# Performance work log

Measured on AMD Instinct MI355X. Metric: run time of the kernel, lower is better.

Reference implementation:

```python
import jax, jax.numpy as jnp
import numpy as np

C, S, D, H, FF = 8, 512, 512, 8, 2048
DH = D // H
N = C * S
NUM_SAMPLES = 4
SEG_LEN = N // NUM_SAMPLES  # 2 channels * 512 tokens per sample


def _ln(x, w, b):
    m = x.mean(-1, keepdims=True)
    v = ((x - m) ** 2).mean(-1, keepdims=True)
    return (x - m) / jnp.sqrt(v + 1e-5) * w + b


def _rope_1d(t, p, inv_freq):
    # t: (H, N, hd), p: (N,), inv_freq: (hd//2,)
    f = p[:, None] * inv_freq[None, :]          # (N, hd//2)
    emb = jnp.concatenate([f, f], -1)           # (N, hd)
    cos, sin = jnp.cos(emb), jnp.sin(emb)
    half = t.shape[-1] // 2
    rot = jnp.concatenate([-t[..., half:], t[..., :half]], -1)
    return t * cos + rot * sin


def setup_inputs() -> dict:
    key = jax.random.key(0)
    ks = jax.random.split(key, 8)
    s = 0.02
    return {
        "x": jax.random.normal(ks[0], (C, S, D), jnp.float32),
        "pos": jax.random.uniform(ks[1], (C, S, 2), jnp.float32) * 100.0,
        "mask": jnp.zeros((C, S), jnp.bool_),
        "seg_ids": jnp.arange(N, dtype=jnp.int32),
        "Wqkv": jax.random.normal(ks[2], (D, 3 * D), jnp.float32) * s,
        "bqkv": jnp.zeros((3 * D,), jnp.float32),
        "Wo": jax.random.normal(ks[3], (D, D), jnp.float32) * s,
        "bo": jnp.zeros((D,), jnp.float32),
        "ln1_w": jnp.ones((D,), jnp.float32),
        "ln1_b": jnp.zeros((D,), jnp.float32),
        "ln2_w": jnp.ones((D,), jnp.float32),
        "ln2_b": jnp.zeros((D,), jnp.float32),
        "W1": jax.random.normal(ks[4], (D, FF), jnp.float32) * s,
        "b1": jnp.zeros((FF,), jnp.float32),
        "W2": jax.random.normal(ks[5], (FF, D), jnp.float32) * s,
        "b2": jnp.zeros((D,), jnp.float32),
    }


def reference(x, pos, mask, seg_ids, Wqkv, bqkv, Wo, bo,
              ln1_w, ln1_b, ln2_w, ln2_b, W1, b1, W2, b2):
    # Zero-mask forward_cc path: all C*S tokens are packed into one varlen batch.
    xf = x.reshape(N, D)
    pf = pos.reshape(N, 2)
    seg = seg_ids // SEG_LEN  # segment id per token (cu_seq_len semantics)

    # --- pre-LN MHA with 2D axial RoPE ---
    hn = _ln(xf, ln1_w, ln1_b)
    qkv = hn @ Wqkv + bqkv
    q, k, v = jnp.split(qkv, 3, axis=-1)
    to_heads = lambda t: t.reshape(N, H, DH).transpose(1, 0, 2)  # (H, N, DH)
    q, k, v = to_heads(q), to_heads(k), to_heads(v)

    hd2 = DH // 2
    inv_freq = 1.0 / (10000.0 ** (jnp.arange(0, hd2, 2, dtype=jnp.float32) / hd2))

    def rope2d(t):
        a = _rope_1d(t[..., :hd2], pf[:, 0], inv_freq)
        b = _rope_1d(t[..., hd2:], pf[:, 1], inv_freq)
        return jnp.concatenate([a, b], -1)

    q, k = rope2d(q), rope2d(k)

    scores = jnp.einsum('hnd,hmd->hnm', q, k) / np.float32(np.sqrt(DH))
    allowed = seg[:, None] == seg[None, :]  # block-diagonal varlen mask
    scores = jnp.where(allowed[None], scores, jnp.float32(-1e30))
    attn = jax.nn.softmax(scores, axis=-1)
    o = jnp.einsum('hnm,hmd->hnd', attn, v).transpose(1, 0, 2).reshape(N, D)
    h = xf + (o @ Wo + bo)

    # --- pre-LN FFN ---
    hn2 = _ln(h, ln2_w, ln2_b)
    h = h + (jax.nn.gelu(hn2 @ W1 + b1) @ W2 + b2)
    return h.reshape(C, S, D)
```

## Files before the change

### kernel.cpp

```cpp
#include <hip/hip_runtime.h>
#include <hip/hip_bf16.h>


typedef __hip_bfloat16 bf16;
typedef float f4 __attribute__((ext_vector_type(4)));
typedef short short8 __attribute__((ext_vector_type(8)));

#define C_ 8
#define S_ 512
#define D_ 512
#define H_ 8
#define DH_ 64
#define FF_ 2048
#define N_ 4096
#define SEGLEN 1024

__device__ __forceinline__ float bfbits2f(unsigned short u) {
    return __uint_as_float(((unsigned)u) << 16);
}
__device__ __forceinline__ unsigned short f2bfbits(float f) {
    __hip_bfloat16 h = __float2bfloat16(f);
    return *reinterpret_cast<unsigned short*>(&h);
}
__device__ __forceinline__ float in_get(const void* p, int i, int isbf) {
    return isbf ? bfbits2f(((const unsigned short*)p)[i]) : ((const float*)p)[i];
}
__device__ __forceinline__ int probe_bf(const void* ln1w) {
    return ((const unsigned*)ln1w)[0] != 0x3F800000u;
}
__device__ __forceinline__ float gelu_f(float x) {
    float u = 0.7978845608028654f * fmaf(0.044715f * x, x * x, x);
    return 0.5f * x * (1.0f + tanhf(u));
}
__device__ __forceinline__ void gl2lds16(const void* g, void* l) {
    __builtin_amdgcn_global_load_lds(
        (const __attribute__((address_space(1))) void*)g,
        (__attribute__((address_space(3))) void*)l, 16, 0, 0);
}

__device__ __forceinline__ void ln_row(
    const void* in, const void* w, const void* b, unsigned short* out,
    int isbf, int row, int lane, int in_fp32)
{
    int base = row * D_ + lane * 8;
    float v[8];
    if (in_fp32 || !isbf) {
        const f4* p = (const f4*)((const float*)in + base);
        f4 x0 = p[0], x1 = p[1];
        v[0] = x0[0]; v[1] = x0[1]; v[2] = x0[2]; v[3] = x0[3];
        v[4] = x1[0]; v[5] = x1[1]; v[6] = x1[2]; v[7] = x1[3];
    } else {
        uint4 u = *(const uint4*)((const unsigned short*)in + base);
        unsigned uu[4] = {u.x, u.y, u.z, u.w};
        #pragma unroll
        for (int j = 0; j < 4; j++) {
            v[2 * j]     = __uint_as_float(uu[j] << 16);
            v[2 * j + 1] = __uint_as_float(uu[j] & 0xFFFF0000u);
        }
    }
    float s = 0.f, q = 0.f;
    #pragma unroll
    for (int j = 0; j < 8; j++) { s += v[j]; q = fmaf(v[j], v[j], q); }
    #pragma unroll
    for (int m = 32; m; m >>= 1) { s += __shfl_xor(s, m); q += __shfl_xor(q, m); }
    float mean = s * (1.f / D_);
    float var  = q * (1.f / D_) - mean * mean;
    float rstd = rsqrtf(var + 1e-5f);
    unsigned short o[8];
    #pragma unroll
    for (int j = 0; j < 8; j++) {
        float wj = in_get(w, lane * 8 + j, isbf);
        float bj = in_get(b, lane * 8 + j, isbf);
        o[j] = f2bfbits((v[j] - mean) * rstd * wj + bj);
    }
    uint4 uo;
    uo.x = o[0] | ((unsigned)o[1] << 16);
    uo.y = o[2] | ((unsigned)o[3] << 16);
    uo.z = o[4] | ((unsigned)o[5] << 16);
    uo.w = o[6] | ((unsigned)o[7] << 16);
    *(uint4*)(out + base) = uo;
}

__global__ __launch_bounds__(256) void prep_kernel(
    const void* __restrict__ Wqkv, const void* __restrict__ Wo,
    const void* __restrict__ W1,   const void* __restrict__ W2,
    bf16* __restrict__ WqkvT, bf16* __restrict__ WoT,
    bf16* __restrict__ W1T,   bf16* __restrict__ W2T,
    const void* __restrict__ x, const void* __restrict__ ln1w,
    const void* __restrict__ ln1b, unsigned short* __restrict__ hn)
{
    const int isbf = probe_bf(ln1w);
    __shared__ unsigned short t2[64 * 40];
    int b = blockIdx.x;
    if (b < 1536) {
        const void* src; bf16* dst; int K, N, nt, kt;
        if (b < 384)       { src = Wqkv; dst = WqkvT; K = 512;  N = 1536; nt = b % 24;          kt = b / 24; }
        else if (b < 512)  { src = Wo;   dst = WoT;   K = 512;  N = 512;  nt = (b - 384) % 8;   kt = (b - 384) / 8; }
        else if (b < 1024) { src = W1;   dst = W1T;   K = 512;  N = 2048; nt = (b - 512) % 32;  kt = (b - 512) / 32; }
        else               { src = W2;   dst = W2T;   K = 2048; N = 512;  nt = (b - 1024) % 8;  kt = (b - 1024) / 8; }
        int nb = nt * 64, kb = kt * 32;
        #pragma unroll
        for (int pass = 0; pass < 2; pass++) {
            int k = pass * 16 + (threadIdx.x >> 4);
            int n = (threadIdx.x & 15) * 4;
            size_t gidx = (size_t)(kb + k) * N + nb + n;
            unsigned short v[4];
            if (!isbf) {
                f4 xv = *(const f4*)((const float*)src + gidx);
                v[0] = f2bfbits(xv[0]); v[1] = f2bfbits(xv[1]);
                v[2] = f2bfbits(xv[2]); v[3] = f2bfbits(xv[3]);
            } else {
                ushort4 u = *(const ushort4*)((const unsigned short*)src + gidx);
                v[0] = u.x; v[1] = u.y; v[2] = u.z; v[3] = u.w;
            }
            #pragma unroll
            for (int e = 0; e < 4; e++) t2[(n + e) * 40 + k] = v[e];
        }
        __syncthreads();
        int n = threadIdx.x >> 2, kc = (threadIdx.x & 3) * 8;
        uint4 w = *(const uint4*)&t2[n * 40 + kc];
        *(uint4*)&((unsigned short*)dst)[(size_t)(nb + n) * K + kb + kc] = w;
    } else {
        int row = (b - 1536) * 4 + (threadIdx.x >> 6);
        ln_row(x, ln1w, ln1b, hn, isbf, row, threadIdx.x & 63, 0);
    }
}

__global__ __launch_bounds__(256) void ln_kernel(
    const void* __restrict__ in, const void* __restrict__ w, const void* __restrict__ b,
    unsigned short* __restrict__ out, const void* __restrict__ dtp, int in_fp32)
{
    const int isbf = probe_bf(dtp);
    int row = blockIdx.x * 4 + (threadIdx.x >> 6);
    ln_row(in, w, b, out, isbf, row, threadIdx.x & 63, in_fp32);
}

template<int MODE, int TN>
__global__ __launch_bounds__(256) void gemm_kernel(
    const bf16* __restrict__ A, const bf16* __restrict__ Bt,
    const void* __restrict__ bias, const void* __restrict__ res,
    const void* __restrict__ pos,
    void* __restrict__ out0, void* __restrict__ out1,
    int K, int NN, const void* __restrict__ dtp)
{
    const int isbf = probe_bf(dtp);
    constexpr int AS = 64 * 64;
    constexpr int BS = TN * 64;
    constexpr int BUF = AS + BS;
    constexpr int VTSZ = 128 * 72;
    constexpr int SMSZ = (2 * BUF > VTSZ) ? 2 * BUF : VTSZ;
    __shared__ __align__(16) unsigned short smem[SMSZ];
    const int X = blockIdx.x & 7, jj = blockIdx.x >> 3;
    const int m0 = ((jj / NN) * 8 + X) * 64;
    const int n0 = (jj % NN) * TN;
    const int tid = threadIdx.x;
    const int wave = tid >> 6, lane = tid & 63;
    const int quad = lane >> 4, l16 = lane & 15;
    const int wr = wave >> 1, wc = wave & 1;
    constexpr int NT = TN / 32;
    constexpr int NB = TN / 32;

    const bf16* gA[2]; int dA[2];
    const bf16* gB[NB]; int dB[NB];
    #pragma unroll
    for (int j = 0; j < 2; j++) {
        int s = j * 256 + tid;
        int r = s >> 3, cc = ((s & 7) - r) & 7;
        gA[j] = A + (size_t)(m0 + r) * K + cc * 8;
        dA[j] = (j * 256 + wave * 64) * 8;
    }
    #pragma unroll
    for (int j = 0; j < NB; j++) {
        int s = j * 256 + tid;
        int r = s >> 3, cc = ((s & 7) - r) & 7;
        gB[j] = Bt + (size_t)(n0 + r) * K + cc * 8;
        dB[j] = (j * 256 + wave * 64) * 8;
    }
    auto stage = [&](int b, int kt) {
        unsigned short* Ab = smem + b * BUF;
        unsigned short* Bb = Ab + AS;
        #pragma unroll
        for (int j = 0; j < 2; j++) gl2lds16(gA[j] + kt * 64, Ab + dA[j]);
        #pragma unroll
        for (int j = 0; j < NB; j++) gl2lds16(gB[j] + kt * 64, Bb + dB[j]);
    };

    f4 acc[2][NT] = {};
    const int nk = K >> 6;
    stage(0, 0);
    #pragma unroll 1
    for (int kt = 0; kt < nk; kt++) {
        const int cur = kt & 1;
        __syncthreads();
        if (kt + 1 < nk) stage(cur ^ 1, kt + 1);
        const unsigned short* Ab = smem + cur * BUF;
        const unsigned short* Bb = Ab + AS;
        short8 af[2][2], bfr[NT][2];
        #pragma unroll
        for (int mi = 0; mi < 2; mi++) {
            int r = wr * 32 + mi * 16 + l16;
            #pragma unroll
            for (int h = 0; h < 2; h++)
                af[mi][h] = *(const short8*)&Ab[(r * 8 + ((h * 4 + quad + r) & 7)) * 8];
        }
        #pragma unroll
        for (int ni = 0; ni < NT; ni++) {
            int r = wc * (TN / 2) + ni * 16 + l16;
            #pragma unroll
            for (int h = 0; h < 2; h++)
                bfr[ni][h] = *(const short8*)&Bb[(r * 8 + ((h * 4 + quad + r) & 7)) * 8];
        }
        #pragma unroll
        for (int mi = 0; mi < 2; mi++)
            #pragma unroll
            for (int ni = 0; ni < NT; ni++) {
                acc[mi][ni] = __builtin_amdgcn_mfma_f32_16x16x32_bf16(af[mi][0], bfr[ni][0], acc[mi][ni], 0, 0, 0);
                acc[mi][ni] = __builtin_amdgcn_mfma_f32_16x16x32_bf16(af[mi][1], bfr[ni][1], acc[mi][ni], 0, 0, 0);
            }
    }

    const int colbase = n0 + wc * (TN / 2);
    float bb[NT];
    #pragma unroll
    for (int ni = 0; ni < NT; ni++) bb[ni] = in_get(bias, colbase + ni * 16 + l16, isbf);

    if (MODE == 1) {
        const int tsel = colbase >> 9;
        const int hd = (colbase & 511) >> 6;
        if (tsel < 2) {
            unsigned short* out = (unsigned short*)out0 + ((size_t)(tsel * H_ + hd) * N_) * 64;
            const float invf = __expf(-(float)l16 * 0.5756462732485114f);
            const float qscale = (tsel == 0) ? 0.125f : 1.0f;
            #pragma unroll
            for (int half = 0; half < 2; half++) {
                #pragma unroll
                for (int mi = 0; mi < 2; mi++) {
                    #pragma unroll
                    for (int r = 0; r < 4; r++) {
                        int row = m0 + wr * 32 + mi * 16 + quad * 4 + r;
                        float p = in_get(pos, row * 2 + half, isbf);
                        float sn, cs;
                        __sincosf(p * invf, &sn, &cs);
                        float v0 = acc[mi][half * 2][r]     + bb[half * 2];
                        float v1 = acc[mi][half * 2 + 1][r] + bb[half * 2 + 1];
                        out[(size_t)row * 64 + half * 32 + l16]      = f2bfbits((v0 * cs - v1 * sn) * qscale);
                        out[(size_t)row * 64 + half * 32 + 16 + l16] = f2bfbits((v1 * cs + v0 * sn) * qscale);
                    }
                }
            }
        } else {
            __syncthreads();
            unsigned short* VT = smem;
            const int vd_blk = n0 - 1024;
            #pragma unroll
            for (int mi = 0; mi < 2; mi++)
                #pragma unroll
                for (int ni = 0; ni < NT; ni++) {
                    int vd = wc * 64 + ni * 16 + l16;
                    #pragma unroll
                    for (int r = 0; r < 4; r++) {
                        int tok = wr * 32 + mi * 16 + quad * 4 + r;
                        VT[vd * 72 + tok] = f2bfbits(acc[mi][ni][r] + bb[ni]);
                    }
                }
            __syncthreads();
            unsigned short* vt = (unsigned short*)out1;
            #pragma unroll
            for (int j = 0; j < 4; j++) {
                int cch = j * 256 + tid;
                int dim = cch >> 3, tc = cch & 7;
                uint4 v = *(const uint4*)&VT[dim * 72 + tc * 8];
                *(uint4*)&vt[(size_t)(vd_blk + dim) * N_ + m0 + tc * 8] = v;
            }
        }
    } else {
        #pragma unroll
        for (int mi = 0; mi < 2; mi++)
            #pragma unroll
            for (int ni = 0; ni < NT; ni++) {
                int col = colbase + ni * 16 + l16;
                #pragma unroll
                for (int r = 0; r < 4; r++) {
                    int row = m0 + wr * 32 + mi * 16 + quad * 4 + r;
                    float val = acc[mi][ni][r] + bb[ni];
                    if (MODE == 2) {
                        size_t idx = (size_t)row * D_ + col;
                        ((float*)out0)[idx] = val + in_get(res, idx, isbf);
                    } else if (MODE == 3) {
                        ((unsigned short*)out0)[(size_t)row * FF_ + col] = f2bfbits(gelu_f(val));
                    } else {
                        size_t idx = (size_t)row * D_ + col;
                        float o = val + ((const float*)res)[idx];
                        if (isbf) ((unsigned short*)out0)[idx] = f2bfbits(o);
                        else      ((float*)out0)[idx] = o;
                    }
                }
            }
    }
}

#define PSTR 136
__global__ __launch_bounds__(256) void attn_kernel(
    const unsigned short* __restrict__ QKb, const unsigned short* __restrict__ Vt,
    unsigned short* __restrict__ ob)
{
    __shared__ __align__(16) unsigned short Ksm[128 * 64];
    __shared__ __align__(16) unsigned short Vsm[64 * 128];
    __shared__ __align__(16) unsigned short Psm[4][16 * PSTR];
    const int h = blockIdx.x & 7, jb = blockIdx.x >> 3;
    const int sg = jb >> 4, qt = jb & 15;
    const int tid = threadIdx.x;
    const int wave = tid >> 6, lane = tid & 63;
    const int quad = lane >> 4, l16 = lane & 15;
    const unsigned short* Qg = QKb + ((size_t)h * N_ + sg * SEGLEN + qt * 64 + wave * 16) * 64;
    const unsigned short* Kg = QKb + ((size_t)(H_ + h) * N_ + sg * SEGLEN) * 64;
    const unsigned short* Vg = Vt + (size_t)h * 64 * N_ + sg * SEGLEN;
    unsigned short* Pw = Psm[wave];

    const unsigned short* gK[4];
    const unsigned short* gV[4];
    unsigned short* lK[4];
    unsigned short* lV[4];
    #pragma unroll
    for (int j = 0; j < 4; j++) {
        int s = j * 256 + tid;
        int rk = s >> 3, ck = ((s & 7) - rk) & 7;
        gK[j] = Kg + (size_t)rk * 64 + ck * 8;
        lK[j] = Ksm + (size_t)(j * 256 + wave * 64) * 8;
        int rv = s >> 4, cv = ((s & 15) - rv) & 15;
        gV[j] = Vg + (size_t)rv * N_ + cv * 8;
        lV[j] = Vsm + (size_t)(j * 256 + wave * 64) * 8;
    }
    const int swzK0 = (quad + l16) & 7;
    const int swzK1 = (4 + quad + l16) & 7;
    int swzV[4];
    #pragma unroll
    for (int kc = 0; kc < 4; kc++) swzV[kc] = (kc * 4 + quad + l16) & 15;

    short8 qf0 = *(const short8*)(Qg + l16 * 64 + quad * 8);
    short8 qf1 = *(const short8*)(Qg + l16 * 64 + 32 + quad * 8);

    f4 o_acc[4] = {};
    float l_part[4] = {0.f, 0.f, 0.f, 0.f};

    #pragma unroll 1
    for (int kt = 0; kt < SEGLEN / 128; kt++) {
        __syncthreads();
        #pragma unroll
        for (int j = 0; j < 4; j++) {
            gl2lds16(gK[j] + (size_t)kt * 128 * 64, lK[j]);
            gl2lds16(gV[j] + kt * 128, lV[j]);
        }
        __syncthreads();

        f4 Sc[8] = {};
        #pragma unroll
        for (int t = 0; t < 8; t++) {
            int r = t * 16 + l16;
            short8 kf0 = *(const short8*)&Ksm[(r * 8 + swzK0) * 8];
            short8 kf1 = *(const short8*)&Ksm[(r * 8 + swzK1) * 8];
            Sc[t] = __builtin_amdgcn_mfma_f32_16x16x32_bf16(qf0, kf0, Sc[t], 0, 0, 0);
            Sc[t] = __builtin_amdgcn_mfma_f32_16x16x32_bf16(qf1, kf1, Sc[t], 0, 0, 0);
        }
        #pragma unroll
        for (int t = 0; t < 8; t++)
            #pragma unroll
            for (int r = 0; r < 4; r++) {
                float pe = __expf(Sc[t][r]);
                Sc[t][r] = pe;
                l_part[r] += pe;
            }
        #pragma unroll
        for (int t = 0; t < 8; t++)
            #pragma unroll
            for (int r = 0; r < 4; r++)
                Pw[(quad * 4 + r) * PSTR + t * 16 + l16] = f2bfbits(Sc[t][r]);
        short8 pf[4];
        #pragma unroll
        for (int kc = 0; kc < 4; kc++)
            pf[kc] = *(const short8*)&Pw[l16 * PSTR + kc * 32 + quad * 8];
        #pragma unroll
        for (int dt = 0; dt < 4; dt++) {
            int r = dt * 16 + l16;
            #pragma unroll
            for (int kc = 0; kc < 4; kc++) {
                short8 vf = *(const short8*)&Vsm[(r * 16 + swzV[kc]) * 8];
                o_acc[dt] = __builtin_amdgcn_mfma_f32_16x16x32_bf16(pf[kc], vf, o_acc[dt], 0, 0, 0);
            }
        }
    }

    #pragma unroll
    for (int r = 0; r < 4; r++) {
        float l = l_part[r];
        l += __shfl_xor(l, 1);
        l += __shfl_xor(l, 2);
        l += __shfl_xor(l, 4);
        l += __shfl_xor(l, 8);
        float inv = 1.0f / l;
        int n = sg * SEGLEN + qt * 64 + wave * 16 + quad * 4 + r;
        #pragma unroll
        for (int dt = 0; dt < 4; dt++)
            ob[(size_t)n * D_ + h * DH_ + dt * 16 + l16] = f2bfbits(o_acc[dt][r] * inv);
    }
}

extern "C" void kernel_launch(void* const* d_in, const int* in_sizes, int n_in,
                              void* d_out, int out_size, void* d_ws, size_t ws_size,
                              hipStream_t stream)
{
    const void* x    = d_in[0];
    const void* pos  = d_in[1];
    const void* Wqkv = d_in[4];
    const void* bqkv = d_in[5];
    const void* Wo   = d_in[6];
    const void* bo   = d_in[7];
    const void* ln1w = d_in[8];
    const void* ln1b = d_in[9];
    const void* ln2w = d_in[10];
    const void* ln2b = d_in[11];
    const void* W1   = d_in[12];
    const void* b1   = d_in[13];
    const void* W2   = d_in[14];
    const void* b2   = d_in[15];

    char* ws = (char*)d_ws;
    size_t off = 0;
    auto take = [&](size_t bytes) -> void* {
        void* p = ws + off;
        off += (bytes + 255) & ~(size_t)255;
        return p;
    };
    bf16* WqkvT           = (bf16*)take((size_t)1536 * 512 * 2);
    bf16* WoT             = (bf16*)take((size_t)512 * 512 * 2);
    bf16* W1T             = (bf16*)take((size_t)2048 * 512 * 2);
    bf16* W2T             = (bf16*)take((size_t)512 * 2048 * 2);
    unsigned short* hn    = (unsigned short*)take((size_t)N_ * D_ * 2);
    unsigned short* QKb   = (unsigned short*)take((size_t)2 * H_ * N_ * DH_ * 2);
    unsigned short* Vtb   = (unsigned short*)take((size_t)H_ * DH_ * N_ * 2);
    unsigned short* obuf  = (unsigned short*)take((size_t)N_ * D_ * 2);
    float* hbuf           = (float*)take((size_t)N_ * D_ * 4);
    unsigned short* hn2   = (unsigned short*)take((size_t)N_ * D_ * 2);
    unsigned short* g     = (unsigned short*)take((size_t)N_ * FF_ * 2);

    prep_kernel<<<1792, 256, 0, stream>>>(
        Wqkv, Wo, W1, W2, WqkvT, WoT, W1T, W2T, x, ln1w, ln1b, hn);

    gemm_kernel<1, 128><<<768, 256, 0, stream>>>(
        (const bf16*)hn, WqkvT, bqkv, nullptr, pos, QKb, Vtb, 512, 12, ln1w);

    attn_kernel<<<512, 256, 0, stream>>>(QKb, Vtb, obuf);

    gemm_kernel<2, 64><<<512, 256, 0, stream>>>(
        (const bf16*)obuf, WoT, bo, x, nullptr, hbuf, nullptr, 512, 8, ln1w);

    ln_kernel<<<N_ / 4, 256, 0, stream>>>(hbuf, ln2w, ln2b, hn2, ln1w, 1);

    gemm_kernel<3, 128><<<1024, 256, 0, stream>>>(
        (const bf16*)hn2, W1T, b1, nullptr, nullptr, g, nullptr, 512, 16, ln1w);

    gemm_kernel<4, 64><<<512, 256, 0, stream>>>(
        (const bf16*)g, W2T, b2, hbuf, nullptr, d_out, nullptr, 2048, 8, ln1w);
}
```

Before: 192.2 us.

## Defer Wo/W1/W2 transposes into QKV GEMM grid and shrink M tile for N=512 GEMMs

The prep kernel now transposes only Wqkv. The Wo, W1 and W2 transpose tiles run as extra blocks appended to the QKV GEMM launch, so that weight preparation overlaps with GEMM work and the prep kernel is shorter. The GEMM kernel gains a TM template parameter, and the Wo-projection and FFN-down GEMMs use 32-row tiles. This doubles their block counts for better CU occupancy, at the cost of less reuse of each B tile. Weights are still transposed on every call, and all consumers of the transposed weights launch after the QKV GEMM.

New measurement: 193.5 us. No clear change (+0.7%).

```diff
diff --git a/kernel.cpp b/kernel.cpp
--- a/kernel.cpp
+++ b/kernel.cpp
@@ -81,47 +81,46 @@
     *(uint4*)(out + base) = uo;
 }
 
+__device__ __forceinline__ void wtile_transpose(
+    const void* __restrict__ src, bf16* __restrict__ dst, int K, int N,
+    int nt, int kt, int isbf, unsigned short* t2)
+{
+    int nb = nt * 64, kb = kt * 32;
+    #pragma unroll
+    for (int pass = 0; pass < 2; pass++) {
+        int k = pass * 16 + (threadIdx.x >> 4);
+        int n = (threadIdx.x & 15) * 4;
+        size_t gidx = (size_t)(kb + k) * N + nb + n;
+        unsigned short v[4];
+        if (!isbf) {
+            f4 xv = *(const f4*)((const float*)src + gidx);
+            v[0] = f2bfbits(xv[0]); v[1] = f2bfbits(xv[1]);
+            v[2] = f2bfbits(xv[2]); v[3] = f2bfbits(xv[3]);
+        } else {
+            ushort4 u = *(const ushort4*)((const unsigned short*)src + gidx);
+            v[0] = u.x; v[1] = u.y; v[2] = u.z; v[3] = u.w;
+        }
+        #pragma unroll
+        for (int e = 0; e < 4; e++) t2[(n + e) * 40 + k] = v[e];
+    }
+    __syncthreads();
+    int n = threadIdx.x >> 2, kc = (threadIdx.x & 3) * 8;
+    uint4 w = *(const uint4*)&t2[n * 40 + kc];
+    *(uint4*)&((unsigned short*)dst)[(size_t)(nb + n) * K + kb + kc] = w;
+}
+
 __global__ __launch_bounds__(256) void prep_kernel(
-    const void* __restrict__ Wqkv, const void* __restrict__ Wo,
-    const void* __restrict__ W1,   const void* __restrict__ W2,
-    bf16* __restrict__ WqkvT, bf16* __restrict__ WoT,
-    bf16* __restrict__ W1T,   bf16* __restrict__ W2T,
+    const void* __restrict__ Wqkv, bf16* __restrict__ WqkvT,
     const void* __restrict__ x, const void* __restrict__ ln1w,
     const void* __restrict__ ln1b, unsigned short* __restrict__ hn)
 {
     const int isbf = probe_bf(ln1w);
     __shared__ unsigned short t2[64 * 40];
     int b = blockIdx.x;
-    if (b < 1536) {
-        const void* src; bf16* dst; int K, N, nt, kt;
-        if (b < 384)       { src = Wqkv; dst = WqkvT; K = 512;  N = 1536; nt = b % 24;          kt = b / 24; }
-        else if (b < 512)  { src = Wo;   dst = WoT;   K = 512;  N = 512;  nt = (b - 384) % 8;   kt = (b - 384) / 8; }
-        else if (b < 1024) { src = W1;   dst = W1T;   K = 512;  N = 2048; nt = (b - 512) % 32;  kt = (b - 512) / 32; }
-        else               { src = W2;   dst = W2T;   K = 2048; N = 512;  nt = (b - 1024) % 8;  kt = (b - 1024) / 8; }
-        int nb = nt * 64, kb = kt * 32;
-        #pragma unroll
-        for (int pass = 0; pass < 2; pass++) {
-            int k = pass * 16 + (threadIdx.x >> 4);
-            int n = (threadIdx.x & 15) * 4;
-            size_t gidx = (size_t)(kb + k) * N + nb + n;
-            unsigned short v[4];
-            if (!isbf) {
-                f4 xv = *(const f4*)((const float*)src + gidx);
-                v[0] = f2bfbits(xv[0]); v[1] = f2bfbits(xv[1]);
-                v[2] = f2bfbits(xv[2]); v[3] = f2bfbits(xv[3]);
-            } else {
-                ushort4 u = *(const ushort4*)((const unsigned short*)src + gidx);
-                v[0] = u.x; v[1] = u.y; v[2] = u.z; v[3] = u.w;
-            }
-            #pragma unroll
-            for (int e = 0; e < 4; e++) t2[(n + e) * 40 + k] = v[e];
-        }
-        __syncthreads();
-        int n = threadIdx.x >> 2, kc = (threadIdx.x & 3) * 8;
-        uint4 w = *(const uint4*)&t2[n * 40 + kc];
-        *(uint4*)&((unsigned short*)dst)[(size_t)(nb + n) * K + kb + kc] = w;
+    if (b < 384) {
+        wtile_transpose(Wqkv, WqkvT, 512, 1536, b % 24, b / 24, isbf, t2);
     } else {
-        int row = (b - 1536) * 4 + (threadIdx.x >> 6);
+        int row = (b - 384) * 4 + (threadIdx.x >> 6);
         ln_row(x, ln1w, ln1b, hn, isbf, row, threadIdx.x & 63, 0);
     }
 }
@@ -135,35 +134,49 @@
     ln_row(in, w, b, out, isbf, row, threadIdx.x & 63, in_fp32);
 }
 
-template<int MODE, int TN>
+template<int MODE, int TM, int TN>
 __global__ __launch_bounds__(256) void gemm_kernel(
     const bf16* __restrict__ A, const bf16* __restrict__ Bt,
     const void* __restrict__ bias, const void* __restrict__ res,
     const void* __restrict__ pos,
     void* __restrict__ out0, void* __restrict__ out1,
-    int K, int NN, const void* __restrict__ dtp)
+    int K, int NN, const void* __restrict__ dtp,
+    const void* __restrict__ tWo, const void* __restrict__ tW1,
+    const void* __restrict__ tW2,
+    bf16* __restrict__ dWo, bf16* __restrict__ dW1, bf16* __restrict__ dW2,
+    int ngemm)
 {
     const int isbf = probe_bf(dtp);
-    constexpr int AS = 64 * 64;
+    constexpr int MI = TM / 32;
+    constexpr int NT = TN / 32;
+    constexpr int NB = TN / 32;
+    constexpr int AS = TM * 64;
     constexpr int BS = TN * 64;
     constexpr int BUF = AS + BS;
     constexpr int VTSZ = 128 * 72;
     constexpr int SMSZ = (2 * BUF > VTSZ) ? 2 * BUF : VTSZ;
     __shared__ __align__(16) unsigned short smem[SMSZ];
+
+    if (MODE == 1 && (int)blockIdx.x >= ngemm) {
+        int t = blockIdx.x - ngemm;
+        if (t < 128)      wtile_transpose(tWo, dWo, 512, 512,  t % 8,  t / 8,  isbf, smem);
+        else if (t < 640) wtile_transpose(tW1, dW1, 512, 2048, (t - 128) % 32, (t - 128) / 32, isbf, smem);
+        else              wtile_transpose(tW2, dW2, 2048, 512, (t - 640) % 8,  (t - 640) / 8,  isbf, smem);
+        return;
+    }
+
     const int X = blockIdx.x & 7, jj = blockIdx.x >> 3;
-    const int m0 = ((jj / NN) * 8 + X) * 64;
+    const int m0 = ((jj / NN) * 8 + X) * TM;
     const int n0 = (jj % NN) * TN;
     const int tid = threadIdx.x;
     const int wave = tid >> 6, lane = tid & 63;
     const int quad = lane >> 4, l16 = lane & 15;
     const int wr = wave >> 1, wc = wave & 1;
-    constexpr int NT = TN / 32;
-    constexpr int NB = TN / 32;
-
-    const bf16* gA[2]; int dA[2];
+
+    const bf16* gA[MI]; int dA[MI];
     const bf16* gB[NB]; int dB[NB];
     #pragma unroll
-    for (int j = 0; j < 2; j++) {
+    for (int j = 0; j < MI; j++) {
         int s = j * 256 + tid;
         int r = s >> 3, cc = ((s & 7) - r) & 7;
         gA[j] = A + (size_t)(m0 + r) * K + cc * 8;
@@ -180,12 +193,12 @@
         unsigned short* Ab = smem + b * BUF;
         unsigned short* Bb = Ab + AS;
         #pragma unroll
-        for (int j = 0; j < 2; j++) gl2lds16(gA[j] + kt * 64, Ab + dA[j]);
+        for (int j = 0; j < MI; j++) gl2lds16(gA[j] + kt * 64, Ab + dA[j]);
         #pragma unroll
         for (int j = 0; j < NB; j++) gl2lds16(gB[j] + kt * 64, Bb + dB[j]);
     };
 
-    f4 acc[2][NT] = {};
+    f4 acc[MI][NT] = {};
     const int nk = K >> 6;
     stage(0, 0);
     #pragma unroll 1
@@ -195,10 +208,10 @@
         if (kt + 1 < nk) stage(cur ^ 1, kt + 1);
         const unsigned short* Ab = smem + cur * BUF;
         const unsigned short* Bb = Ab + AS;
-        short8 af[2][2], bfr[NT][2];
-        #pragma unroll
-        for (int mi = 0; mi < 2; mi++) {
-            int r = wr * 32 + mi * 16 + l16;
+        short8 af[MI][2], bfr[NT][2];
+        #pragma unroll
+        for (int mi = 0; mi < MI; mi++) {
+            int r = wr * (TM / 2) + mi * 16 + l16;
             #pragma unroll
             for (int h = 0; h < 2; h++)
                 af[mi][h] = *(const short8*)&Ab[(r * 8 + ((h * 4 + quad + r) & 7)) * 8];
@@ -211,7 +224,7 @@
                 bfr[ni][h] = *(const short8*)&Bb[(r * 8 + ((h * 4 + quad + r) & 7)) * 8];
         }
         #pragma unroll
-        for (int mi = 0; mi < 2; mi++)
+        for (int mi = 0; mi < MI; mi++)
             #pragma unroll
             for (int ni = 0; ni < NT; ni++) {
                 acc[mi][ni] = __builtin_amdgcn_mfma_f32_16x16x32_bf16(af[mi][0], bfr[ni][0], acc[mi][ni], 0, 0, 0);
@@ -234,10 +247,10 @@
             #pragma unroll
             for (int half = 0; half < 2; half++) {
                 #pragma unroll
-                for (int mi = 0; mi < 2; mi++) {
+                for (int mi = 0; mi < MI; mi++) {
                     #pragma unroll
                     for (int r = 0; r < 4; r++) {
-                        int row = m0 + wr * 32 + mi * 16 + quad * 4 + r;
+                        int row = m0 + wr * (TM / 2) + mi * 16 + quad * 4 + r;
                         float p = in_get(pos, row * 2 + half, isbf);
                         float sn, cs;
                         __sincosf(p * invf, &sn, &cs);
@@ -253,13 +266,13 @@
             unsigned short* VT = smem;
             const int vd_blk = n0 - 1024;
             #pragma unroll
-            for (int mi = 0; mi < 2; mi++)
+            for (int mi = 0; mi < MI; mi++)
                 #pragma unroll
                 for (int ni = 0; ni < NT; ni++) {
                     int vd = wc * 64 + ni * 16 + l16;
                     #pragma unroll
                     for (int r = 0; r < 4; r++) {
-                        int tok = wr * 32 + mi * 16 + quad * 4 + r;
+                        int tok = wr * (TM / 2) + mi * 16 + quad * 4 + r;
                         VT[vd * 72 + tok] = f2bfbits(acc[mi][ni][r] + bb[ni]);
                     }
                 }
@@ -275,13 +288,13 @@
         }
     } else {
         #pragma unroll
-        for (int mi = 0; mi < 2; mi++)
+        for (int mi = 0; mi < MI; mi++)
             #pragma unroll
             for (int ni = 0; ni < NT; ni++) {
                 int col = colbase + ni * 16 + l16;
                 #pragma unroll
                 for (int r = 0; r < 4; r++) {
-                    int row = m0 + wr * 32 + mi * 16 + quad * 4 + r;
+                    int row = m0 + wr * (TM / 2) + mi * 16 + quad * 4 + r;
                     float val = acc[mi][ni][r] + bb[ni];
                     if (MODE == 2) {
                         size_t idx = (size_t)row * D_ + col;
@@ -443,22 +456,25 @@
     unsigned short* hn2   = (unsigned short*)take((size_t)N_ * D_ * 2);
     unsigned short* g     = (unsigned short*)take((size_t)N_ * FF_ * 2);
 
-    prep_kernel<<<1792, 256, 0, stream>>>(
-        Wqkv, Wo, W1, W2, WqkvT, WoT, W1T, W2T, x, ln1w, ln1b, hn);
-
-    gemm_kernel<1, 128><<<768, 256, 0, stream>>>(
-        (const bf16*)hn, WqkvT, bqkv, nullptr, pos, QKb, Vtb, 512, 12, ln1w);
+    prep_kernel<<<1408, 256, 0, stream>>>(Wqkv, WqkvT, x, ln1w, ln1b, hn);
+
+    gemm_kernel<1, 64, 128><<<1920, 256, 0, stream>>>(
+        (const bf16*)hn, WqkvT, bqkv, nullptr, pos, QKb, Vtb, 512, 12, ln1w,
+        Wo, W1, W2, WoT, W1T, W2T, 768);
 
     attn_kernel<<<512, 256, 0, stream>>>(QKb, Vtb, obuf);
 
-    gemm_kernel<2, 64><<<512, 256, 0, stream>>>(
-        (const bf16*)obuf, WoT, bo, x, nullptr, hbuf, nullptr, 512, 8, ln1w);
+    gemm_kernel<2, 32, 64><<<1024, 256, 0, stream>>>(
+        (const bf16*)obuf, WoT, bo, x, nullptr, hbuf, nullptr, 512, 8, ln1w,
+        nullptr, nullptr, nullptr, nullptr, nullptr, nullptr, 1 << 30);
 
     ln_kernel<<<N_ / 4, 256, 0, stream>>>(hbuf, ln2w, ln2b, hn2, ln1w, 1);
 
-    gemm_kernel<3, 128><<<1024, 256, 0, stream>>>(
-        (const bf16*)hn2, W1T, b1, nullptr, nullptr, g, nullptr, 512, 16, ln1w);
-
-    gemm_kernel<4, 64><<<512, 256, 0, stream>>>(
-        (const bf16*)g, W2T, b2, hbuf, nullptr, d_out, nullptr, 2048, 8, ln1w);
-}
+    gemm_kernel<3, 64, 128><<<1024, 256, 0, stream>>>(
+        (const bf16*)hn2, W1T, b1, nullptr, nullptr, g, nullptr, 512, 16, ln1w,
+        nullptr, nullptr, nullptr, nullptr, nullptr, nullptr, 1 << 30);
+
+    gemm_kernel<4, 32, 64><<<1024, 256, 0, stream>>>(
+        (const bf16*)g, W2T, b2, hbuf, nullptr, d_out, nullptr, 2048, 8, ln1w,
+        nullptr, nullptr, nullptr, nullptr, nullptr, nullptr, 1 << 30);
+}
```
